# Performance work log

Hardware: AMD Instinct MI355X
Metric: run time of the kernel (lower is better)

Reference implementation:

```python
import jax, jax.numpy as jnp
import numpy as np

N = 50000
E = 600000
D = 128
HEADS = 4
G = 64  # num graphs
EPS = 1e-5


def setup_inputs() -> dict:
    key = jax.random.key(0)
    ks = jax.random.split(key, 16)
    s = 0.05
    inp = {
        'x': jax.random.normal(ks[0], (N, D), jnp.float32),
        'edge_index': jax.random.randint(ks[1], (2, E), 0, N, jnp.int64),
        'batch': jnp.sort(jax.random.randint(ks[2], (N,), 0, G, jnp.int64)),
        # GCN layer 1
        'W1': jax.random.normal(ks[3], (D, D), jnp.float32) * s,
        'b1': jnp.zeros((D,), jnp.float32),
        'g1': jnp.ones((D,), jnp.float32),
        'beta1': jnp.zeros((D,), jnp.float32),
        # GCN layer 2
        'W2': jax.random.normal(ks[4], (D, D), jnp.float32) * s,
        'b2': jnp.zeros((D,), jnp.float32),
        'g2': jnp.ones((D,), jnp.float32),
        'beta2': jnp.zeros((D,), jnp.float32),
        # GAT (heads=4, concat=False -> mean over heads)
        'gat_W': jax.random.normal(ks[5], (D, HEADS * D), jnp.float32) * s,
        'att_src': jax.random.normal(ks[6], (HEADS, D), jnp.float32) * s,
        'att_dst': jax.random.normal(ks[7], (HEADS, D), jnp.float32) * s,
        'gat_b': jnp.zeros((D,), jnp.float32),
    }
    return inp


def _layer_norm(x, g, b):
    mu = jnp.mean(x, axis=-1, keepdims=True)
    var = jnp.mean((x - mu) ** 2, axis=-1, keepdims=True)
    return (x - mu) * jax.lax.rsqrt(var + EPS) * g + b


def _gcn(x, W, b, src, dst, deg_inv_sqrt):
    h = x @ W                                    # [N, D]
    norm = deg_inv_sqrt[src] * deg_inv_sqrt[dst]  # [E']
    msg = norm[:, None] * h[src]                 # [E', D] gather
    return jax.ops.segment_sum(msg, dst, num_segments=N) + b


def _gat(x, W, b, att_src, att_dst, src, dst):
    h = (x @ W).reshape(N, HEADS, D)             # [N, H, D]
    a_s = jnp.einsum('nhd,hd->nh', h, att_src)   # [N, H]
    a_d = jnp.einsum('nhd,hd->nh', h, att_dst)
    e = jax.nn.leaky_relu(a_s[src] + a_d[dst], 0.2)          # [E', H]
    m = jax.ops.segment_max(e, dst, num_segments=N)          # segment softmax
    ex = jnp.exp(e - m[dst])
    den = jax.ops.segment_sum(ex, dst, num_segments=N)
    alpha = ex / den[dst]                                     # [E', H]
    out = jax.ops.segment_sum(alpha[:, :, None] * h[src], dst, num_segments=N)
    return jnp.mean(out, axis=1) + b             # concat=False -> head mean


def reference(x, edge_index, batch, W1, b1, g1, beta1, W2, b2, g2, beta2,
              gat_W, gat_b, att_src, att_dst):
    # add self loops (PyG default for GCNConv and GATConv)
    loops = jnp.arange(N, dtype=edge_index.dtype)
    src = jnp.concatenate([edge_index[0], loops])
    dst = jnp.concatenate([edge_index[1], loops])
    deg = jax.ops.segment_sum(jnp.ones_like(dst, jnp.float32), dst, num_segments=N)
    deg_inv_sqrt = jnp.where(deg > 0, jax.lax.rsqrt(jnp.maximum(deg, 1.0)), 0.0)

    # GCN stack: conv -> LayerNorm -> relu -> dropout(eval=identity)
    h = jax.nn.relu(_layer_norm(_gcn(x, W1, b1, src, dst, deg_inv_sqrt), g1, beta1))
    h = jax.nn.relu(_layer_norm(_gcn(h, W2, b2, src, dst, deg_inv_sqrt), g2, beta2))

    h = jax.nn.relu(_gat(h, gat_W, gat_b, att_src, att_dst, src, dst))
    node_embeddings = h

    cnt = jax.ops.segment_sum(jnp.ones((N,), jnp.float32), batch, num_segments=G)
    mean_pool = jax.ops.segment_sum(h, batch, num_segments=G) / jnp.maximum(cnt, 1.0)[:, None]
    max_pool = jax.ops.segment_max(h, batch, num_segments=G)
    graph_embedding = jnp.concatenate([mean_pool, max_pool], axis=1)  # [G, 2D]
    return graph_embedding, node_embeddings
```

## Files before the change

### kernel.cpp

```cpp
#include <hip/hip_runtime.h>
#include <math.h>


#define TPB 256

typedef __attribute__((ext_vector_type(8))) short short8;
typedef __attribute__((ext_vector_type(4))) float f32x4;
union U4S8 { uint4 u; short8 s; };

__device__ __forceinline__ float lrelu(float x) { return x > 0.f ? x : 0.2f * x; }

__device__ __forceinline__ unsigned short f2bf(float f) {
    unsigned int u = __float_as_uint(f);
    u += 0x7fffu + ((u >> 16) & 1u);
    return (unsigned short)(u >> 16);
}
__device__ __forceinline__ float2 bf2x(unsigned int u) {
    return make_float2(__uint_as_float(u << 16), __uint_as_float(u & 0xffff0000u));
}
__device__ __forceinline__ float sel4(float4 v, int h) {
    float r = v.x;
    r = (h == 1) ? v.y : r;
    r = (h == 2) ? v.z : r;
    r = (h == 3) ? v.w : r;
    return r;
}
__device__ __forceinline__ float dot4(f32x4 a, float4 b) {
    return a.x * b.x + a.y * b.y + a.z * b.z + a.w * b.w;
}

__global__ __launch_bounds__(TPB) void k_hist(const int* __restrict__ dst,
                                              int* __restrict__ deg, int e) {
    int i = blockIdx.x * TPB + threadIdx.x;
    if (i < e) atomicAdd(&deg[dst[i]], 1);
}

__global__ __launch_bounds__(TPB) void k_scan_part_wt(const int* __restrict__ deg,
                                                      int* __restrict__ part, int n, int nb,
                                                      const float* __restrict__ W1,
                                                      const float* __restrict__ W2,
                                                      const float* __restrict__ Wg,
                                                      unsigned short* __restrict__ Wt1,
                                                      unsigned short* __restrict__ Wt2,
                                                      unsigned short* __restrict__ Wtg) {
    int bid = blockIdx.x;
    if (bid < nb) {
        int i = bid * TPB + threadIdx.x;
        int v = (i < n) ? deg[i] : 0;
#pragma unroll
        for (int o = 32; o > 0; o >>= 1) v += __shfl_xor(v, o);
        __shared__ int sw[4];
        if ((threadIdx.x & 63) == 0) sw[threadIdx.x >> 6] = v;
        __syncthreads();
        if (threadIdx.x == 0) part[bid] = sw[0] + sw[1] + sw[2] + sw[3];
    } else {
        int i = (bid - nb) * TPB + threadIdx.x;
        if (i < 16384) {
            int k = i >> 7, c = i & 127;
            Wt1[c * 128 + k] = f2bf(W1[i]);
        } else if (i < 32768) {
            int j = i - 16384;
            int k = j >> 7, c = j & 127;
            Wt2[c * 128 + k] = f2bf(W2[j]);
        } else if (i < 98304) {
            int j = i - 32768;
            int k = j >> 9, c = j & 511;
            Wtg[c * 128 + k] = f2bf(Wg[j]);
        }
    }
}

__global__ __launch_bounds__(TPB) void k_scan_apply(const int* __restrict__ deg,
                                                    const int* __restrict__ part,
                                                    int* __restrict__ row_start,
                                                    int* __restrict__ cursor,
                                                    float* __restrict__ dis,
                                                    int n, int e_total) {
    __shared__ int sm[TPB];
    __shared__ int sred[4];
    int t = threadIdx.x;
    int bid = blockIdx.x;
    int pv = (t < bid) ? part[t] : 0;
#pragma unroll
    for (int o = 32; o > 0; o >>= 1) pv += __shfl_xor(pv, o);
    if ((t & 63) == 0) sred[t >> 6] = pv;
    __syncthreads();
    int basep = sred[0] + sred[1] + sred[2] + sred[3];
    int i = bid * TPB + t;
    int d = (i < n) ? deg[i] : 0;
    sm[t] = d;
    __syncthreads();
    for (int off = 1; off < TPB; off <<= 1) {
        int u = (t >= off) ? sm[t - off] : 0;
        __syncthreads();
        sm[t] += u;
        __syncthreads();
    }
    if (i < n) {
        int rs = basep + sm[t] - d;
        row_start[i] = rs;
        cursor[i] = rs;
        dis[i] = rsqrtf((float)(d + 1));
    }
    if (bid == 0 && t == 0) row_start[n] = e_total;
}

__global__ __launch_bounds__(TPB) void k_scatter(const int* __restrict__ src,
                                                 const int* __restrict__ dst,
                                                 int* __restrict__ cursor,
                                                 int* __restrict__ csr_src, int e) {
    int i = blockIdx.x * TPB + threadIdx.x;
    if (i < e) {
        int p = atomicAdd(&cursor[dst[i]], 1);
        csr_src[p] = src[i];
    }
}

__global__ __launch_bounds__(TPB, 2) void k_gemm_mfma(const unsigned short* __restrict__ feat,
                                                      const unsigned short* __restrict__ Wt,
                                                      unsigned short* __restrict__ C,
                                                      int nrows, int ocols,
                                                      const float* __restrict__ att_s,
                                                      const float* __restrict__ att_d,
                                                      float* __restrict__ a_s,
                                                      float* __restrict__ a_d) {
    __shared__ uint4 wl[2048];
    __shared__ float sas[128], sad[128];
    int t = threadIdx.x;
    int cb = blockIdx.y << 7;
#pragma unroll
    for (int i = 0; i < 8; ++i) {
        int fi = i * 256 + t;
        int l = fi & 63, ct = (fi >> 6) & 7, ks = fi >> 9;
        int chan = cb + ct * 16 + (l & 15);
        wl[fi] = ((const uint4*)(Wt + (size_t)chan * 128))[ks * 4 + (l >> 4)];
    }
    __syncthreads();

    int wave = t >> 6, lane = t & 63;
    int wr = wave >> 1, wc = wave & 1;
    int nbase = (blockIdx.x << 7) + (wc << 6);
    const uint4* brow[4];
#pragma unroll
    for (int nt = 0; nt < 4; ++nt) {
        int node = nbase + nt * 16 + (lane & 15);
        node = node < nrows ? node : (nrows - 1);
        brow[nt] = (const uint4*)(feat + (size_t)node * 128);
    }
    f32x4 acc[4][4];
#pragma unroll
    for (int mt = 0; mt < 4; ++mt)
#pragma unroll
        for (int nt = 0; nt < 4; ++nt) acc[mt][nt] = (f32x4)0.f;

    int kq = lane >> 4;
#pragma unroll
    for (int ks = 0; ks < 4; ++ks) {
        U4S8 a[4], b[4];
#pragma unroll
        for (int mt = 0; mt < 4; ++mt)
            a[mt].u = wl[(ks * 8 + wr * 4 + mt) * 64 + lane];
#pragma unroll
        for (int nt = 0; nt < 4; ++nt)
            b[nt].u = brow[nt][ks * 4 + kq];
#pragma unroll
        for (int mt = 0; mt < 4; ++mt)
#pragma unroll
            for (int nt = 0; nt < 4; ++nt)
                acc[mt][nt] = __builtin_amdgcn_mfma_f32_16x16x32_bf16(
                    a[mt].s, b[nt].s, acc[mt][nt], 0, 0, 0);
    }
#pragma unroll
    for (int nt = 0; nt < 4; ++nt) {
        int node = nbase + nt * 16 + (lane & 15);
        if (node >= nrows) continue;
#pragma unroll
        for (int mt = 0; mt < 4; ++mt) {
            int chan = cb + (wr << 6) + mt * 16 + (lane >> 4) * 4;
            f32x4 v = acc[mt][nt];
            unsigned int p0 = (unsigned int)f2bf(v.x) | ((unsigned int)f2bf(v.y) << 16);
            unsigned int p1 = (unsigned int)f2bf(v.z) | ((unsigned int)f2bf(v.w) << 16);
            *(uint2*)(C + (size_t)node * ocols + chan) = make_uint2(p0, p1);
        }
    }
    if (att_s) {
        if (t < 128) { sas[t] = 0.f; sad[t] = 0.f; }
        __syncthreads();
        int h = blockIdx.y;
        float4 asv[4], adv[4];
#pragma unroll
        for (int mt = 0; mt < 4; ++mt) {
            int cbase = h * 128 + (wr << 6) + mt * 16 + (lane >> 4) * 4;
            asv[mt] = *(const float4*)(att_s + cbase);
            adv[mt] = *(const float4*)(att_d + cbase);
        }
#pragma unroll
        for (int nt = 0; nt < 4; ++nt) {
            float ds = 0.f, dd = 0.f;
#pragma unroll
            for (int mt = 0; mt < 4; ++mt) {
                ds += dot4(acc[mt][nt], asv[mt]);
                dd += dot4(acc[mt][nt], adv[mt]);
            }
            ds += __shfl_xor(ds, 16); ds += __shfl_xor(ds, 32);
            dd += __shfl_xor(dd, 16); dd += __shfl_xor(dd, 32);
            if (lane < 16) {
                atomicAdd(&sas[(wc << 6) + nt * 16 + lane], ds);
                atomicAdd(&sad[(wc << 6) + nt * 16 + lane], dd);
            }
        }
        __syncthreads();
        if (t < 128) {
            int node = (blockIdx.x << 7) + t;
            if (node < nrows) a_s[node * 4 + h] = sas[t];
        } else {
            int t2 = t - 128;
            int node = (blockIdx.x << 7) + t2;
            if (node < nrows) a_d[node * 4 + h] = sad[t2];
        }
    }
}

__global__ __launch_bounds__(TPB, 2) void k_gemm_mfma_f32(const float* __restrict__ feat,
                                                          const unsigned short* __restrict__ Wt,
                                                          unsigned short* __restrict__ C,
                                                          int nrows, int ocols) {
    __shared__ uint4 wl[2048];
    int t = threadIdx.x;
    int cb = blockIdx.y << 7;
#pragma unroll
    for (int i = 0; i < 8; ++i) {
        int fi = i * 256 + t;
        int l = fi & 63, ct = (fi >> 6) & 7, ks = fi >> 9;
        int chan = cb + ct * 16 + (l & 15);
        wl[fi] = ((const uint4*)(Wt + (size_t)chan * 128))[ks * 4 + (l >> 4)];
    }
    __syncthreads();

    int wave = t >> 6, lane = t & 63;
    int wr = wave >> 1, wc = wave & 1;
    int nbase = (blockIdx.x << 7) + (wc << 6);
    const float4* brow[4];
#pragma unroll
    for (int nt = 0; nt < 4; ++nt) {
        int node = nbase + nt * 16 + (lane & 15);
        node = node < nrows ? node : (nrows - 1);
        brow[nt] = (const float4*)(feat + (size_t)node * 128);
    }
    f32x4 acc[4][4];
#pragma unroll
    for (int mt = 0; mt < 4; ++mt)
#pragma unroll
        for (int nt = 0; nt < 4; ++nt) acc[mt][nt] = (f32x4)0.f;

    int kq = lane >> 4;
#pragma unroll
    for (int ks = 0; ks < 4; ++ks) {
        U4S8 a[4], b[4];
#pragma unroll
        for (int mt = 0; mt < 4; ++mt)
            a[mt].u = wl[(ks * 8 + wr * 4 + mt) * 64 + lane];
#pragma unroll
        for (int nt = 0; nt < 4; ++nt) {
            float4 f0 = brow[nt][ks * 8 + kq * 2];
            float4 f1 = brow[nt][ks * 8 + kq * 2 + 1];
            b[nt].u.x = (unsigned int)f2bf(f0.x) | ((unsigned int)f2bf(f0.y) << 16);
            b[nt].u.y = (unsigned int)f2bf(f0.z) | ((unsigned int)f2bf(f0.w) << 16);
            b[nt].u.z = (unsigned int)f2bf(f1.x) | ((unsigned int)f2bf(f1.y) << 16);
            b[nt].u.w = (unsigned int)f2bf(f1.z) | ((unsigned int)f2bf(f1.w) << 16);
        }
#pragma unroll
        for (int mt = 0; mt < 4; ++mt)
#pragma unroll
            for (int nt = 0; nt < 4; ++nt)
                acc[mt][nt] = __builtin_amdgcn_mfma_f32_16x16x32_bf16(
                    a[mt].s, b[nt].s, acc[mt][nt], 0, 0, 0);
    }
#pragma unroll
    for (int nt = 0; nt < 4; ++nt) {
        int node = nbase + nt * 16 + (lane & 15);
        if (node >= nrows) continue;
#pragma unroll
        for (int mt = 0; mt < 4; ++mt) {
            int chan = cb + (wr << 6) + mt * 16 + (lane >> 4) * 4;
            f32x4 v = acc[mt][nt];
            unsigned int p0 = (unsigned int)f2bf(v.x) | ((unsigned int)f2bf(v.y) << 16);
            unsigned int p1 = (unsigned int)f2bf(v.z) | ((unsigned int)f2bf(v.w) << 16);
            *(uint2*)(C + (size_t)node * ocols + chan) = make_uint2(p0, p1);
        }
    }
}

__global__ __launch_bounds__(TPB) void k_gcn_fused(const unsigned short* __restrict__ hb,
                                                   const int* __restrict__ csr_src,
                                                   const int* __restrict__ row_start,
                                                   const float* __restrict__ dis,
                                                   const float* __restrict__ b,
                                                   const float* __restrict__ g,
                                                   const float* __restrict__ beta,
                                                   unsigned short* __restrict__ out, int n) {
    int node = (blockIdx.x * TPB + threadIdx.x) >> 6;
    int lane = threadIdx.x & 63;
    if (node >= n) return;
    int s0 = row_start[node], s1 = row_start[node + 1];
    float dn = dis[node];
    const uint4* hq = (const uint4*)hb;
    int q = lane >> 4, fl = lane & 15;
    float acc[8];
#pragma unroll
    for (int i = 0; i < 8; ++i) acc[i] = 0.f;
    for (int base = s0; base < s1; base += 64) {
        int cnt = min(64, s1 - base);
        int sidx = 0; float w = 0.f;
        if (lane < cnt) { sidx = csr_src[base + lane]; w = dis[sidx]; }
        for (int j = 0; j < cnt; j += 16) {
            int j0 = j + q, j1 = j + 4 + q, j2 = j + 8 + q, j3 = j + 12 + q;
            int   sA = __shfl(sidx, j0), sB = __shfl(sidx, j1);
            int   sC = __shfl(sidx, j2), sD = __shfl(sidx, j3);
            float wA = __shfl(w, j0), wB = __shfl(w, j1);
            float wC = __shfl(w, j2), wD = __shfl(w, j3);
            uint4 uA = hq[(size_t)sA * 16 + fl];
            uint4 uB = hq[(size_t)sB * 16 + fl];
            uint4 uC = hq[(size_t)sC * 16 + fl];
            uint4 uD = hq[(size_t)sD * 16 + fl];
            float2 p0 = bf2x(uA.x), p1 = bf2x(uA.y), p2 = bf2x(uA.z), p3 = bf2x(uA.w);
            acc[0] += wA * p0.x; acc[1] += wA * p0.y;
            acc[2] += wA * p1.x; acc[3] += wA * p1.y;
            acc[4] += wA * p2.x; acc[5] += wA * p2.y;
            acc[6] += wA * p3.x; acc[7] += wA * p3.y;
            p0 = bf2x(uB.x); p1 = bf2x(uB.y); p2 = bf2x(uB.z); p3 = bf2x(uB.w);
            acc[0] += wB * p0.x; acc[1] += wB * p0.y;
            acc[2] += wB * p1.x; acc[3] += wB * p1.y;
            acc[4] += wB * p2.x; acc[5] += wB * p2.y;
            acc[6] += wB * p3.x; acc[7] += wB * p3.y;
            p0 = bf2x(uC.x); p1 = bf2x(uC.y); p2 = bf2x(uC.z); p3 = bf2x(uC.w);
            acc[0] += wC * p0.x; acc[1] += wC * p0.y;
            acc[2] += wC * p1.x; acc[3] += wC * p1.y;
            acc[4] += wC * p2.x; acc[5] += wC * p2.y;
            acc[6] += wC * p3.x; acc[7] += wC * p3.y;
            p0 = bf2x(uD.x); p1 = bf2x(uD.y); p2 = bf2x(uD.z); p3 = bf2x(uD.w);
            acc[0] += wD * p0.x; acc[1] += wD * p0.y;
            acc[2] += wD * p1.x; acc[3] += wD * p1.y;
            acc[4] += wD * p2.x; acc[5] += wD * p2.y;
            acc[6] += wD * p3.x; acc[7] += wD * p3.y;
        }
    }
#pragma unroll
    for (int i = 0; i < 8; ++i) {
        acc[i] += __shfl_xor(acc[i], 16);
        acc[i] += __shfl_xor(acc[i], 32);
    }
    float sl = dn * dn;
    uint4 us = hq[(size_t)node * 16 + fl];
    float2 h0 = bf2x(us.x), h1 = bf2x(us.y), h2 = bf2x(us.z), h3 = bf2x(us.w);
    float4 b0 = ((const float4*)b)[fl * 2], b1 = ((const float4*)b)[fl * 2 + 1];
    float v[8];
    v[0] = dn * acc[0] + sl * h0.x + b0.x;
    v[1] = dn * acc[1] + sl * h0.y + b0.y;
    v[2] = dn * acc[2] + sl * h1.x + b0.z;
    v[3] = dn * acc[3] + sl * h1.y + b0.w;
    v[4] = dn * acc[4] + sl * h2.x + b1.x;
    v[5] = dn * acc[5] + sl * h2.y + b1.y;
    v[6] = dn * acc[6] + sl * h3.x + b1.z;
    v[7] = dn * acc[7] + sl * h3.y + b1.w;
    float s = 0.f, sq = 0.f;
#pragma unroll
    for (int i = 0; i < 8; ++i) { s += v[i]; sq += v[i] * v[i]; }
#pragma unroll
    for (int o = 8; o > 0; o >>= 1) {
        s  += __shfl_xor(s, o);
        sq += __shfl_xor(sq, o);
    }
    float mu = s * (1.f / 128.f);
    float var = sq * (1.f / 128.f) - mu * mu;
    float rstd = rsqrtf(var + 1e-5f);
    float4 g0  = ((const float4*)g)[fl * 2],    g1v = ((const float4*)g)[fl * 2 + 1];
    float4 bt0 = ((const float4*)beta)[fl * 2], bt1 = ((const float4*)beta)[fl * 2 + 1];
    float o0 = fmaxf((v[0] - mu) * rstd * g0.x + bt0.x, 0.f);
    float o1 = fmaxf((v[1] - mu) * rstd * g0.y + bt0.y, 0.f);
    float o2 = fmaxf((v[2] - mu) * rstd * g0.z + bt0.z, 0.f);
    float o3 = fmaxf((v[3] - mu) * rstd * g0.w + bt0.w, 0.f);
    float o4 = fmaxf((v[4] - mu) * rstd * g1v.x + bt1.x, 0.f);
    float o5 = fmaxf((v[5] - mu) * rstd * g1v.y + bt1.y, 0.f);
    float o6 = fmaxf((v[6] - mu) * rstd * g1v.z + bt1.z, 0.f);
    float o7 = fmaxf((v[7] - mu) * rstd * g1v.w + bt1.w, 0.f);
    if (q == 0) {
        uint4 pk;
        pk.x = (unsigned int)f2bf(o0) | ((unsigned int)f2bf(o1) << 16);
        pk.y = (unsigned int)f2bf(o2) | ((unsigned int)f2bf(o3) << 16);
        pk.z = (unsigned int)f2bf(o4) | ((unsigned int)f2bf(o5) << 16);
        pk.w = (unsigned int)f2bf(o6) | ((unsigned int)f2bf(o7) << 16);
        ((uint4*)out)[(size_t)node * 16 + fl] = pk;
    }
}

__global__ __launch_bounds__(TPB) void k_gat_fused(const unsigned short* __restrict__ hgb,
                                                   const float* __restrict__ a_s,
                                                   const float* __restrict__ a_d,
                                                   const int* __restrict__ csr_src,
                                                   const int* __restrict__ row_start,
                                                   const float* __restrict__ gat_b,
                                                   float* __restrict__ node_out, int n) {
    __shared__ int   ssrc[4][64];
    __shared__ float swt[4][4][65];
    int node = (blockIdx.x * TPB + threadIdx.x) >> 6;
    int lane = threadIdx.x & 63;
    int wid = threadIdx.x >> 6;
    if (node >= n) return;
    int s0 = row_start[node], s1 = row_start[node + 1];
    int h = lane >> 4;
    const float4* as4 = (const float4*)a_s;
    float4 ad = ((const float4*)a_d)[node];
    float4 asn = as4[node];
    float4 wself;
    wself.x = __expf(lrelu(asn.x + ad.x));
    wself.y = __expf(lrelu(asn.y + ad.y));
    wself.z = __expf(lrelu(asn.z + ad.z));
    wself.w = __expf(lrelu(asn.w + ad.w));
    const uint4* hq = (const uint4*)hgb;
    float acc[8];
    {
        float wsh = sel4(wself, h);
        uint4 u = hq[(size_t)node * 64 + lane];
        float2 p0 = bf2x(u.x), p1 = bf2x(u.y), p2 = bf2x(u.z), p3 = bf2x(u.w);
        acc[0] = wsh * p0.x; acc[1] = wsh * p0.y;
        acc[2] = wsh * p1.x; acc[3] = wsh * p1.y;
        acc[4] = wsh * p2.x; acc[5] = wsh * p2.y;
        acc[6] = wsh * p3.x; acc[7] = wsh * p3.y;
    }
    float4 den = make_float4(0.f, 0.f, 0.f, 0.f);
    for (int base = s0; base < s1; base += 64) {
        int cnt = min(64, s1 - base);
        int sidx = 0;
        float4 w4 = make_float4(0.f, 0.f, 0.f, 0.f);
        if (lane < cnt) {
            sidx = csr_src[base + lane];
            float4 a = as4[sidx];
            w4.x = __expf(lrelu(a.x + ad.x));
            w4.y = __expf(lrelu(a.y + ad.y));
            w4.z = __expf(lrelu(a.z + ad.z));
            w4.w = __expf(lrelu(a.w + ad.w));
            den.x += w4.x; den.y += w4.y; den.z += w4.z; den.w += w4.w;
        }
        ssrc[wid][lane] = sidx;
        swt[wid][0][lane] = w4.x;
        swt[wid][1][lane] = w4.y;
        swt[wid][2][lane] = w4.z;
        swt[wid][3][lane] = w4.w;
        int j = 0;
        for (; j + 4 <= cnt; j += 4) {
            int sa = ssrc[wid][j + 0], sb = ssrc[wid][j + 1];
            int sc = ssrc[wid][j + 2], sd = ssrc[wid][j + 3];
            float wa = swt[wid][h][j + 0], wb = swt[wid][h][j + 1];
            float wc = swt[wid][h][j + 2], wd = swt[wid][h][j + 3];
            uint4 ua = hq[(size_t)sa * 64 + lane];
            uint4 ub = hq[(size_t)sb * 64 + lane];
            uint4 uc = hq[(size_t)sc * 64 + lane];
            uint4 ud = hq[(size_t)sd * 64 + lane];
            float2 p0, p1, p2, p3;
            p0 = bf2x(ua.x); p1 = bf2x(ua.y); p2 = bf2x(ua.z); p3 = bf2x(ua.w);
            acc[0] += wa * p0.x; acc[1] += wa * p0.y; acc[2] += wa * p1.x; acc[3] += wa * p1.y;
            acc[4] += wa * p2.x; acc[5] += wa * p2.y; acc[6] += wa * p3.x; acc[7] += wa * p3.y;
            p0 = bf2x(ub.x); p1 = bf2x(ub.y); p2 = bf2x(ub.z); p3 = bf2x(ub.w);
            acc[0] += wb * p0.x; acc[1] += wb * p0.y; acc[2] += wb * p1.x; acc[3] += wb * p1.y;
            acc[4] += wb * p2.x; acc[5] += wb * p2.y; acc[6] += wb * p3.x; acc[7] += wb * p3.y;
            p0 = bf2x(uc.x); p1 = bf2x(uc.y); p2 = bf2x(uc.z); p3 = bf2x(uc.w);
            acc[0] += wc * p0.x; acc[1] += wc * p0.y; acc[2] += wc * p1.x; acc[3] += wc * p1.y;
            acc[4] += wc * p2.x; acc[5] += wc * p2.y; acc[6] += wc * p3.x; acc[7] += wc * p3.y;
            p0 = bf2x(ud.x); p1 = bf2x(ud.y); p2 = bf2x(ud.z); p3 = bf2x(ud.w);
            acc[0] += wd * p0.x; acc[1] += wd * p0.y; acc[2] += wd * p1.x; acc[3] += wd * p1.y;
            acc[4] += wd * p2.x; acc[5] += wd * p2.y; acc[6] += wd * p3.x; acc[7] += wd * p3.y;
        }
        for (; j < cnt; ++j) {
            int s = ssrc[wid][j];
            float wj = swt[wid][h][j];
            uint4 u = hq[(size_t)s * 64 + lane];
            float2 p0 = bf2x(u.x), p1 = bf2x(u.y), p2 = bf2x(u.z), p3 = bf2x(u.w);
            acc[0] += wj * p0.x; acc[1] += wj * p0.y;
            acc[2] += wj * p1.x; acc[3] += wj * p1.y;
            acc[4] += wj * p2.x; acc[5] += wj * p2.y;
            acc[6] += wj * p3.x; acc[7] += wj * p3.y;
        }
    }
#pragma unroll
    for (int o = 32; o > 0; o >>= 1) {
        den.x += __shfl_xor(den.x, o);
        den.y += __shfl_xor(den.y, o);
        den.z += __shfl_xor(den.z, o);
        den.w += __shfl_xor(den.w, o);
    }
    den.x += wself.x; den.y += wself.y; den.z += wself.z; den.w += wself.w;
    float winv = 0.25f / sel4(den, h);
#pragma unroll
    for (int j = 0; j < 8; ++j) acc[j] *= winv;
#pragma unroll
    for (int j = 0; j < 8; ++j) acc[j] += __shfl_xor(acc[j], 16);
#pragma unroll
    for (int j = 0; j < 8; ++j) acc[j] += __shfl_xor(acc[j], 32);
    int fl = lane & 15;
    float4 gb0 = ((const float4*)gat_b)[fl * 2], gb1 = ((const float4*)gat_b)[fl * 2 + 1];
    if (lane < 16) {
        float4* o4 = (float4*)(node_out + (size_t)node * 128 + fl * 8);
        o4[0] = make_float4(fmaxf(acc[0] + gb0.x, 0.f), fmaxf(acc[1] + gb0.y, 0.f),
                            fmaxf(acc[2] + gb0.z, 0.f), fmaxf(acc[3] + gb0.w, 0.f));
        o4[1] = make_float4(fmaxf(acc[4] + gb1.x, 0.f), fmaxf(acc[5] + gb1.y, 0.f),
                            fmaxf(acc[6] + gb1.z, 0.f), fmaxf(acc[7] + gb1.w, 0.f));
    }
}

__global__ __launch_bounds__(TPB) void k_pool(const float* __restrict__ node_out,
                                              const int* __restrict__ batch,
                                              float* __restrict__ mean_acc,
                                              float* __restrict__ max_acc,
                                              float* __restrict__ cnt, int n) {
    int wave = (blockIdx.x * TPB + threadIdx.x) >> 6;
    int lane = threadIdx.x & 63;
    int n0 = wave * 16;
    if (n0 >= n) return;
    int n1 = min(n0 + 16, n);
    float2 bsum = make_float2(0.f, 0.f), bmax = make_float2(0.f, 0.f);
    int cur_g = batch[n0];
    int cntloc = 0;
    for (int nn = n0; nn < n1; ++nn) {
        int g = batch[nn];
        if (g != cur_g) {
            float* ma = mean_acc + cur_g * 128 + lane * 2;
            atomicAdd(ma + 0, bsum.x);
            atomicAdd(ma + 1, bsum.y);
            int* mxp = (int*)(max_acc + cur_g * 128 + lane * 2);
            atomicMax(mxp + 0, __float_as_int(bmax.x));
            atomicMax(mxp + 1, __float_as_int(bmax.y));
            if (lane == 0) atomicAdd(&cnt[cur_g], (float)cntloc);
            bsum = make_float2(0.f, 0.f);
            bmax = make_float2(0.f, 0.f);
            cntloc = 0;
            cur_g = g;
        }
        float2 o = ((const float2*)node_out)[(size_t)nn * 64 + lane];
        bsum.x += o.x; bsum.y += o.y;
        bmax.x = fmaxf(bmax.x, o.x); bmax.y = fmaxf(bmax.y, o.y);
        ++cntloc;
    }
    float* ma = mean_acc + cur_g * 128 + lane * 2;
    atomicAdd(ma + 0, bsum.x);
    atomicAdd(ma + 1, bsum.y);
    int* mxp = (int*)(max_acc + cur_g * 128 + lane * 2);
    atomicMax(mxp + 0, __float_as_int(bmax.x));
    atomicMax(mxp + 1, __float_as_int(bmax.y));
    if (lane == 0) atomicAdd(&cnt[cur_g], (float)cntloc);
}

__global__ __launch_bounds__(TPB) void k_pool_final(const float* __restrict__ mean_acc,
                                                    const float* __restrict__ max_acc,
                                                    const float* __restrict__ cnt,
                                                    float* __restrict__ gout, int g128) {
    int i = blockIdx.x * TPB + threadIdx.x;
    if (i >= g128) return;
    int g = i >> 7, d = i & 127;
    float c = fmaxf(cnt[g], 1.f);
    gout[g * 256 + d] = mean_acc[i] / c;
    gout[g * 256 + 128 + d] = max_acc[i];
}

extern "C" void kernel_launch(void* const* d_in, const int* in_sizes, int n_in,
                              void* d_out, int out_size, void* d_ws, size_t ws_size,
                              hipStream_t stream) {
    const float* x       = (const float*)d_in[0];
    const int*   ei      = (const int*)d_in[1];
    const int*   batch   = (const int*)d_in[2];
    const float* W1      = (const float*)d_in[3];
    const float* b1      = (const float*)d_in[4];
    const float* g1      = (const float*)d_in[5];
    const float* beta1   = (const float*)d_in[6];
    const float* W2      = (const float*)d_in[7];
    const float* b2      = (const float*)d_in[8];
    const float* g2      = (const float*)d_in[9];
    const float* beta2   = (const float*)d_in[10];
    const float* gat_W   = (const float*)d_in[11];
    const float* att_src = (const float*)d_in[12];
    const float* att_dst = (const float*)d_in[13];
    const float* gat_b   = (const float*)d_in[14];

    const int N = in_sizes[0] / 128;
    const int E = in_sizes[1] / 2;
    const int G = (out_size - N * 128) / 256;
    const int* src = ei;
    const int* dst = ei + E;

    float* ws = (float*)d_ws;
    float* dis      = ws; ws += N;
    float* a_s      = ws; ws += N * 4;
    float* a_d      = ws; ws += N * 4;
    float* mean_acc = ws; ws += G * 128;
    float* max_acc  = ws; ws += G * 128;
    float* cnt      = ws; ws += G;
    unsigned short* Hbf = (unsigned short*)ws; ws += (size_t)N * 64;
    unsigned short* Bbf = (unsigned short*)ws; ws += (size_t)N * 64;
    unsigned short* Cbf = (unsigned short*)ws; ws += (size_t)N * 64;
    unsigned short* hgb = (unsigned short*)ws; ws += (size_t)N * 256;
    unsigned short* Wt1 = (unsigned short*)ws; ws += 128 * 64;
    unsigned short* Wt2 = (unsigned short*)ws; ws += 128 * 64;
    unsigned short* Wtg = (unsigned short*)ws; ws += 512 * 64;
    int* deg       = (int*)ws; ws += N;
    int* part      = (int*)ws; ws += 256;
    int* row_start = (int*)ws; ws += N + 1;
    int* cursor    = (int*)ws; ws += N + 1;
    int* csr_src   = (int*)ws; ws += E;

    float* gout = (float*)d_out;
    float* node_out = gout + G * 256;

    auto cdiv = [](long a, long b) { return (int)((a + b - 1) / b); };
    const int nb = cdiv(N, TPB);

    hipMemsetAsync(deg, 0, (size_t)N * 4, stream);
    k_hist<<<cdiv(E, TPB), TPB, 0, stream>>>(dst, deg, E);
    k_scan_part_wt<<<nb + cdiv(98304, TPB), TPB, 0, stream>>>(deg, part, N, nb,
                                                              W1, W2, gat_W, Wt1, Wt2, Wtg);
    k_scan_apply<<<nb, TPB, 0, stream>>>(deg, part, row_start, cursor, dis, N, E);
    k_scatter<<<cdiv(E, TPB), TPB, 0, stream>>>(src, dst, cursor, csr_src, E);

    k_gemm_mfma_f32<<<dim3(cdiv(N, 128), 1), TPB, 0, stream>>>(x, Wt1, Hbf, N, 128);
    k_gcn_fused<<<cdiv((long)N * 64, TPB), TPB, 0, stream>>>(Hbf, csr_src, row_start, dis,
                                                             b1, g1, beta1, Bbf, N);
    k_gemm_mfma<<<dim3(cdiv(N, 128), 1), TPB, 0, stream>>>(Bbf, Wt2, Hbf, N, 128,
                                                           nullptr, nullptr, nullptr, nullptr);
    k_gcn_fused<<<cdiv((long)N * 64, TPB), TPB, 0, stream>>>(Hbf, csr_src, row_start, dis,
                                                             b2, g2, beta2, Cbf, N);
    k_gemm_mfma<<<dim3(cdiv(N, 128), 4), TPB, 0, stream>>>(Cbf, Wtg, hgb, N, 512,
                                                           att_src, att_dst, a_s, a_d);
    k_gat_fused<<<cdiv((long)N * 64, TPB), TPB, 0, stream>>>(hgb, a_s, a_d, csr_src, row_start,
                                                             gat_b, node_out, N);

    hipMemsetAsync(mean_acc, 0, (size_t)(G * 256 + G) * 4, stream);
    k_pool<<<cdiv((long)cdiv(N, 16) * 64, TPB), TPB, 0, stream>>>(node_out, batch,
                                                                  mean_acc, max_acc, cnt, N);
    k_pool_final<<<cdiv((long)G * 128, TPB), TPB, 0, stream>>>(mean_acc, max_acc, cnt, gout, G * 128);
}
```

Baseline: 424.1 us.

## Fuse edge scatter into first GEMM launch and precompute per-edge source weights

Merges the CSR scatter kernel and the first f32-input GEMM into one launch, with extra blocks doing the scatter so both run concurrently. The scatter now also stores dis[src] per CSR entry, so the GCN aggregation reads a contiguous weight array instead of doing a dependent gather on dis. The two memsets are combined into one by moving deg next to the pooling accumulators. This trades extra per-edge weight storage and a mixed-role kernel for fewer launches and fewer dependent loads.

```diff
diff --git a/kernel.cpp b/kernel.cpp
--- a/kernel.cpp
+++ b/kernel.cpp
@@ -105,14 +105,88 @@
     if (bid == 0 && t == 0) row_start[n] = e_total;
 }
 
-__global__ __launch_bounds__(TPB) void k_scatter(const int* __restrict__ src,
-                                                 const int* __restrict__ dst,
-                                                 int* __restrict__ cursor,
-                                                 int* __restrict__ csr_src, int e) {
-    int i = blockIdx.x * TPB + threadIdx.x;
-    if (i < e) {
-        int p = atomicAdd(&cursor[dst[i]], 1);
-        csr_src[p] = src[i];
+__global__ __launch_bounds__(TPB, 2) void k_gemm1_scatter(const float* __restrict__ feat,
+                                                          const unsigned short* __restrict__ Wt,
+                                                          unsigned short* __restrict__ C,
+                                                          int nrows, int gb,
+                                                          const int* __restrict__ src,
+                                                          const int* __restrict__ dst,
+                                                          const float* __restrict__ dis,
+                                                          int* __restrict__ cursor,
+                                                          int* __restrict__ csr_src,
+                                                          float* __restrict__ csr_w, int e) {
+    __shared__ uint4 wl[2048];
+    int t = threadIdx.x;
+    if (blockIdx.x >= gb) {
+        int i = (blockIdx.x - gb) * TPB + t;
+        if (i < e) {
+            int s = src[i];
+            int p = atomicAdd(&cursor[dst[i]], 1);
+            csr_src[p] = s;
+            csr_w[p] = dis[s];
+        }
+        return;
+    }
+#pragma unroll
+    for (int i = 0; i < 8; ++i) {
+        int fi = i * 256 + t;
+        int l = fi & 63, ct = (fi >> 6) & 7, ks = fi >> 9;
+        int chan = ct * 16 + (l & 15);
+        wl[fi] = ((const uint4*)(Wt + (size_t)chan * 128))[ks * 4 + (l >> 4)];
+    }
+    __syncthreads();
+
+    int wave = t >> 6, lane = t & 63;
+    int wr = wave >> 1, wc = wave & 1;
+    int nbase = (blockIdx.x << 7) + (wc << 6);
+    const float4* brow[4];
+#pragma unroll
+    for (int nt = 0; nt < 4; ++nt) {
+        int node = nbase + nt * 16 + (lane & 15);
+        node = node < nrows ? node : (nrows - 1);
+        brow[nt] = (const float4*)(feat + (size_t)node * 128);
+    }
+    f32x4 acc[4][4];
+#pragma unroll
+    for (int mt = 0; mt < 4; ++mt)
+#pragma unroll
+        for (int nt = 0; nt < 4; ++nt) acc[mt][nt] = (f32x4)0.f;
+
+    int kq = lane >> 4;
+#pragma unroll
+    for (int ks = 0; ks < 4; ++ks) {
+        U4S8 a[4], b[4];
+#pragma unroll
+        for (int mt = 0; mt < 4; ++mt)
+            a[mt].u = wl[(ks * 8 + wr * 4 + mt) * 64 + lane];
+#pragma unroll
+        for (int nt = 0; nt < 4; ++nt) {
+            float4 f0 = brow[nt][ks * 8 + kq * 2];
+            float4 f1 = brow[nt][ks * 8 + kq * 2 + 1];
+            b[nt].u.x = (unsigned int)f2bf(f0.x) | ((unsigned int)f2bf(f0.y) << 16);
+            b[nt].u.y = (unsigned int)f2bf(f0.z) | ((unsigned int)f2bf(f0.w) << 16);
+            b[nt].u.z = (unsigned int)f2bf(f1.x) | ((unsigned int)f2bf(f1.y) << 16);
+            b[nt].u.w = (unsigned int)f2bf(f1.z) | ((unsigned int)f2bf(f1.w) << 16);
+        }
+#pragma unroll
+        for (int mt = 0; mt < 4; ++mt)
+#pragma unroll
+            for (int nt = 0; nt < 4; ++nt)
+                acc[mt][nt] = __builtin_amdgcn_mfma_f32_16x16x32_bf16(
+                    a[mt].s, b[nt].s, acc[mt][nt], 0, 0, 0);
+    }
+#pragma unroll
+    for (int nt = 0; nt < 4; ++nt) {
+        int node = nbase + nt * 16 + (lane & 15);
+        if (node >= nrows) continue;
+#pragma unroll
+        for (int mt = 0; mt < 4; ++mt) {
+            int chan = (wr << 6) + mt * 16 + (lane >> 4) * 4;
+            f32x4 v = acc[mt][nt];
+            unsigned int p0 = (unsigned int)f2bf(v.x) | ((unsigned int)f2bf(v.y) << 16);
+            unsigned int p1 = (unsigned int)f2bf(v.z) | ((unsigned int)f2bf(v.w) << 16);
+            *(uint2*)(C + (size_t)node * 128 + chan) = make_uint2(p0, p1);
+        }
     }
 }
 
@@ -221,78 +295,9 @@
     }
 }
 
-__global__ __launch_bounds__(TPB, 2) void k_gemm_mfma_f32(const float* __restrict__ feat,
-                                                          const unsigned short* __restrict__ Wt,
-                                                          unsigned short* __restrict__ C,
-                                                          int nrows, int ocols) {
-    __shared__ uint4 wl[2048];
-    int t = threadIdx.x;
-    int cb = blockIdx.y << 7;
-#pragma unroll
-    for (int i = 0; i < 8; ++i) {
-        int fi = i * 256 + t;
-        int l = fi & 63, ct = (fi >> 6) & 7, ks = fi >> 9;
-        int chan = cb + ct * 16 + (l & 15);
-        wl[fi] = ((const uint4*)(Wt + (size_t)chan * 128))[ks * 4 + (l >> 4)];
-    }
-    __syncthreads();
-
-    int wave = t >> 6, lane = t & 63;
-    int wr = wave >> 1, wc = wave & 1;
-    int nbase = (blockIdx.x << 7) + (wc << 6);
-    const float4* brow[4];
-#pragma unroll
-    for (int nt = 0; nt < 4; ++nt) {
-        int node = nbase + nt * 16 + (lane & 15);
-        node = node < nrows ? node : (nrows - 1);
-        brow[nt] = (const float4*)(feat + (size_t)node * 128);
-    }
-    f32x4 acc[4][4];
-#pragma unroll
-    for (int mt = 0; mt < 4; ++mt)
-#pragma unroll
-        for (int nt = 0; nt < 4; ++nt) acc[mt][nt] = (f32x4)0.f;
-
-    int kq = lane >> 4;
-#pragma unroll
-    for (int ks = 0; ks < 4; ++ks) {
-        U4S8 a[4], b[4];
-#pragma unroll
-        for (int mt = 0; mt < 4; ++mt)
-            a[mt].u = wl[(ks * 8 + wr * 4 + mt) * 64 + lane];
-#pragma unroll
-        for (int nt = 0; nt < 4; ++nt) {
-            float4 f0 = brow[nt][ks * 8 + kq * 2];
-            float4 f1 = brow[nt][ks * 8 + kq * 2 + 1];
-            b[nt].u.x = (unsigned int)f2bf(f0.x) | ((unsigned int)f2bf(f0.y) << 16);
-            b[nt].u.y = (unsigned int)f2bf(f0.z) | ((unsigned int)f2bf(f0.w) << 16);
-            b[nt].u.z = (unsigned int)f2bf(f1.x) | ((unsigned int)f2bf(f1.y) << 16);
-            b[nt].u.w = (unsigned int)f2bf(f1.z) | ((unsigned int)f2bf(f1.w) << 16);
-        }
-#pragma unroll
-        for (int mt = 0; mt < 4; ++mt)
-#pragma unroll
-            for (int nt = 0; nt < 4; ++nt)
-                acc[mt][nt] = __builtin_amdgcn_mfma_f32_16x16x32_bf16(
-                    a[mt].s, b[nt].s, acc[mt][nt], 0, 0, 0);
-    }
-#pragma unroll
-    for (int nt = 0; nt < 4; ++nt) {
-        int node = nbase + nt * 16 + (lane & 15);
-        if (node >= nrows) continue;
-#pragma unroll
-        for (int mt = 0; mt < 4; ++mt) {
-            int chan = cb + (wr << 6) + mt * 16 + (lane >> 4) * 4;
-            f32x4 v = acc[mt][nt];
-            unsigned int p0 = (unsigned int)f2bf(v.x) | ((unsigned int)f2bf(v.y) << 16);
-            unsigned int p1 = (unsigned int)f2bf(v.z) | ((unsigned int)f2bf(v.w) << 16);
-            *(uint2*)(C + (size_t)node * ocols + chan) = make_uint2(p0, p1);
-        }
-    }
-}
-
 __global__ __launch_bounds__(TPB) void k_gcn_fused(const unsigned short* __restrict__ hb,
                                                    const int* __restrict__ csr_src,
+                                                   const float* __restrict__ csr_w,
                                                    const int* __restrict__ row_start,
                                                    const float* __restrict__ dis,
                                                    const float* __restrict__ b,
@@ -312,7 +317,10 @@
     for (int base = s0; base < s1; base += 64) {
         int cnt = min(64, s1 - base);
         int sidx = 0; float w = 0.f;
-        if (lane < cnt) { sidx = csr_src[base + lane]; w = dis[sidx]; }
+        if (lane < cnt) {
+            sidx = csr_src[base + lane];
+            w = csr_w[base + lane];
+        }
         for (int j = 0; j < cnt; j += 16) {
             int j0 = j + q, j1 = j + 4 + q, j2 = j + 8 + q, j3 = j + 12 + q;
             int   sA = __shfl(sidx, j0), sB = __shfl(sidx, j1);
@@ -594,6 +602,8 @@
     float* mean_acc = ws; ws += G * 128;
     float* max_acc  = ws; ws += G * 128;
     float* cnt      = ws; ws += G;
+    int* deg        = (int*)ws; ws += N;
+    float* csr_w    = ws; ws += E;
     unsigned short* Hbf = (unsigned short*)ws; ws += (size_t)N * 64;
     unsigned short* Bbf = (unsigned short*)ws; ws += (size_t)N * 64;
     unsigned short* Cbf = (unsigned short*)ws; ws += (size_t)N * 64;
@@ -601,7 +611,6 @@
     unsigned short* Wt1 = (unsigned short*)ws; ws += 128 * 64;
     unsigned short* Wt2 = (unsigned short*)ws; ws += 128 * 64;
     unsigned short* Wtg = (unsigned short*)ws; ws += 512 * 64;
-    int* deg       = (int*)ws; ws += N;
     int* part      = (int*)ws; ws += 256;
     int* row_start = (int*)ws; ws += N + 1;
     int* cursor    = (int*)ws; ws += N + 1;
@@ -613,26 +622,27 @@
     auto cdiv = [](long a, long b) { return (int)((a + b - 1) / b); };
     const int nb = cdiv(N, TPB);
 
-    hipMemsetAsync(deg, 0, (size_t)N * 4, stream);
+    hipMemsetAsync(mean_acc, 0, (size_t)(G * 256 + G + N) * 4, stream);
     k_hist<<<cdiv(E, TPB), TPB, 0, stream>>>(dst, deg, E);
     k_scan_part_wt<<<nb + cdiv(98304, TPB), TPB, 0, stream>>>(deg, part, N, nb,
                                                               W1, W2, gat_W, Wt1, Wt2, Wtg);
     k_scan_apply<<<nb, TPB, 0, stream>>>(deg, part, row_start, cursor, dis, N, E);
-    k_scatter<<<cdiv(E, TPB), TPB, 0, stream>>>(src, dst, cursor, csr_src, E);
-
-    k_gemm_mfma_f32<<<dim3(cdiv(N, 128), 1), TPB, 0, stream>>>(x, Wt1, Hbf, N, 128);
-    k_gcn_fused<<<cdiv((long)N * 64, TPB), TPB, 0, stream>>>(Hbf, csr_src, row_start, dis,
+
+    const int gb = cdiv(N, 128);
+    k_gemm1_scatter<<<gb + cdiv(E, TPB), TPB, 0, stream>>>(x, Wt1, Hbf, N, gb,
+                                                           src, dst, dis, cursor,
+                                                           csr_src, csr_w, E);
+    k_gcn_fused<<<cdiv((long)N * 64, TPB), TPB, 0, stream>>>(Hbf, csr_src, csr_w, row_start, dis,
                                                              b1, g1, beta1, Bbf, N);
     k_gemm_mfma<<<dim3(cdiv(N, 128), 1), TPB, 0, stream>>>(Bbf, Wt2, Hbf, N, 128,
                                                            nullptr, nullptr, nullptr, nullptr);
-    k_gcn_fused<<<cdiv((long)N * 64, TPB), TPB, 0, stream>>>(Hbf, csr_src, row_start, dis,
+    k_gcn_fused<<<cdiv((long)N * 64, TPB), TPB, 0, stream>>>(Hbf, csr_src, csr_w, row_start, dis,
                                                              b2, g2, beta2, Cbf, N);
     k_gemm_mfma<<<dim3(cdiv(N, 128), 4), TPB, 0, stream>>>(Cbf, Wtg, hgb, N, 512,
                                                            att_src, att_dst, a_s, a_d);
     k_gat_fused<<<cdiv((long)N * 64, TPB), TPB, 0, stream>>>(hgb, a_s, a_d, csr_src, row_start,
                                                              gat_b, node_out, N);
 
-    hipMemsetAsync(mean_acc, 0, (size_t)(G * 256 + G) * 4, stream);
     k_pool<<<cdiv((long)cdiv(N, 16) * 64, TPB), TPB, 0, stream>>>(node_out, batch,
                                                                   mean_acc, max_acc, cnt, N);
     k_pool_final<<<cdiv((long)G * 128, TPB), TPB, 0, stream>>>(mean_acc, max_acc, cnt, gout, G * 128);
```

Measured after the change: 407.2 us. 4.0% less time.
